# Optimization experiments

Hardware: AMD Instinct MI355X
Metric: run time of the kernel (lower is better)

The kernel has to match this reference:

```python
import jax, jax.numpy as jnp
import numpy as np


def _pairwise_dist(A, B):
    # Euclidean cdist via ||a||^2 + ||b||^2 - 2 a.b, avoiding a [B,N,M,D] intermediate.
    a2 = jnp.sum(A * A, axis=-1)  # [b, n]
    b2 = jnp.sum(B * B, axis=-1)  # [b, m]
    ab = jnp.einsum('bnd,bmd->bnm', A, B)  # [b, n, m]
    sq = a2[:, :, None] + b2[:, None, :] - 2.0 * ab
    return jnp.sqrt(jnp.maximum(sq, 0.0))


def setup_inputs() -> dict:
    key = jax.random.key(0)
    kA, kB = jax.random.split(key)
    A = jax.random.normal(kA, (4, 8192, 3), dtype=jnp.float32)
    B = jax.random.normal(kB, (4, 8192, 3), dtype=jnp.float32)
    return {"A": A, "B": B}


def reference(A, B):
    d = _pairwise_dist(A, B)              # [b, n, m]
    min_a2b = jnp.min(d, axis=2)          # [b, n]
    min_b2a = jnp.min(d, axis=1)          # [b, m]
    chamfer = jnp.mean(min_a2b, axis=1) + jnp.mean(min_b2a, axis=1)  # [b]
    return jnp.mean(chamfer) / 12.8
```

## Files before the change

### kernel.cpp

```cpp
#include <hip/hip_runtime.h>


typedef __bf16 bf16x8 __attribute__((ext_vector_type(8)));
typedef float f32x16 __attribute__((ext_vector_type(16)));
typedef unsigned short u16;

constexpr int NB = 4;
constexpr int NPTS = 8192;
constexpr int NROWS = 2 * NB * NPTS;
constexpr int FRAGS = 8;
constexpr int ROWS_PER_BLK = FRAGS * 32;
constexpr int ROWBLKS = NPTS / ROWS_PER_BLK;
constexpr int SSPLIT = 4;
constexpr int SPTS = NPTS / SSPLIT;
constexpr int TILES_PER_WAVE = SPTS / 32 / 4;
constexpr int DEPTH = 4;

constexpr size_t REST_OFF = 2u << 20;
constexpr size_t WSMIN_OFF = 4u << 20;

__device__ __forceinline__ float bsplit(float x, u16& hbits, float& hf) {
    unsigned u = __float_as_uint(x);
    unsigned r = (u + 0x7FFFu + ((u >> 16) & 1u)) & 0xFFFF0000u;
    hbits = (u16)(r >> 16);
    hf = __uint_as_float(r);
    return x - hf;
}

__global__ __launch_bounds__(256)
void chamfer_prep_kernel(const float* __restrict__ A, const float* __restrict__ B,
                         u16* __restrict__ streamT, u16* __restrict__ resT,
                         unsigned int* __restrict__ ws_min) {
    int idx = blockIdx.x * 256 + threadIdx.x;
    int pt = idx & (NPTS - 1);
    int batch = (idx >> 13) & (NB - 1);
    int set = idx >> 15;
    const float* src = (set ? B : A) + ((size_t)batch * NPTS + pt) * 3;
    float x = src[0], y = src[1], z = src[2];
    float s2 = fmaf(x, x, fmaf(y, y, z * z));
    float hf, h2;
    u16 s2h, s2l, s2ll, xh, xl, yh, yl, zh, zl, mxh, mxl, myh, myl, mzh, mzl;
    float r1 = bsplit(s2, s2h, hf);
    float r2 = bsplit(r1, s2l, h2);
    bsplit(r2, s2ll, h2);
    float t;
    t = bsplit(x, xh, hf);          bsplit(t, xl, h2);
    t = bsplit(y, yh, hf);          bsplit(t, yl, h2);
    t = bsplit(z, zh, hf);          bsplit(t, zl, h2);
    t = bsplit(-2.0f * x, mxh, hf); bsplit(t, mxl, h2);
    t = bsplit(-2.0f * y, myh, hf); bsplit(t, myl, h2);
    t = bsplit(-2.0f * z, mzh, hf); bsplit(t, mzl, h2);
    const unsigned ONE = 0x3F80u;
    #define PK(a, b) ((unsigned)(a) | ((unsigned)(b) << 16))
    uint4 rw0 = make_uint4(PK(s2h, s2l), PK(s2ll, ONE), PK(ONE, ONE), PK(mxh, myh));
    uint4 rw1 = make_uint4(PK(mzh, mxh), PK(myh, mzh), PK(mxl, myl), PK(mzl, 0));
    uint4 cw0 = make_uint4(PK(ONE, ONE), PK(ONE, s2h), PK(s2l, s2ll), PK(xh, yh));
    uint4 cw1 = make_uint4(PK(zh, xl), PK(yl, zl), PK(xh, yh), PK(zh, 0));
    #undef PK
    uint4* sp = (uint4*)(streamT + (size_t)idx * 16);
    uint4* rp = (uint4*)(resT + (size_t)idx * 16);
    sp[0] = rw0; sp[1] = rw1;
    rp[0] = cw0; rp[1] = cw1;
    ws_min[idx] = 0xFFFFFFFFu;
}

__device__ __forceinline__ float tree16acc(const f32x16& d, float acc) {
    float m0 = fminf(fminf(d[0],  d[1]),  d[2]);
    float m1 = fminf(fminf(d[3],  d[4]),  d[5]);
    float m2 = fminf(fminf(d[6],  d[7]),  d[8]);
    float m3 = fminf(fminf(d[9],  d[10]), d[11]);
    float m4 = fminf(fminf(d[12], d[13]), d[14]);
    float n0 = fminf(fminf(m0, m1), m2);
    float n1 = fminf(fminf(m3, m4), d[15]);
    return fminf(fminf(n0, n1), acc);
}

__global__ __launch_bounds__(256, 4)
void chamfer_minmfma_kernel(const u16* __restrict__ streamT,
                            const u16* __restrict__ resT,
                            unsigned int* __restrict__ ws_min) {
    int db     = blockIdx.x & 7;
    int rest   = blockIdx.x >> 3;
    int split  = rest & (SSPLIT - 1);
    int rowblk = rest >> 2;
    int batch  = db & (NB - 1);
    int dir    = db >> 2;

    int lane = threadIdx.x & 63;
    int wave = threadIdx.x >> 6;
    int l31 = lane & 31, lh = lane >> 5;

    const u16* rbase = resT + (((size_t)(dir * NB + batch) * NPTS) + rowblk * ROWS_PER_BLK) * 16;
    bf16x8 res0 = *(const bf16x8*)(rbase + (0 * 32 + l31) * 16 + lh * 8);
    bf16x8 res1 = *(const bf16x8*)(rbase + (1 * 32 + l31) * 16 + lh * 8);
    bf16x8 res2 = *(const bf16x8*)(rbase + (2 * 32 + l31) * 16 + lh * 8);
    bf16x8 res3 = *(const bf16x8*)(rbase + (3 * 32 + l31) * 16 + lh * 8);
    bf16x8 res4 = *(const bf16x8*)(rbase + (4 * 32 + l31) * 16 + lh * 8);
    bf16x8 res5 = *(const bf16x8*)(rbase + (5 * 32 + l31) * 16 + lh * 8);
    bf16x8 res6 = *(const bf16x8*)(rbase + (6 * 32 + l31) * 16 + lh * 8);
    bf16x8 res7 = *(const bf16x8*)(rbase + (7 * 32 + l31) * 16 + lh * 8);

    const uint4* wp = (const uint4*)streamT
                    + (size_t)((dir ^ 1) * NB + batch) * NPTS * 2
                    + (size_t)split * SPTS * 2
                    + (size_t)wave * TILES_PER_WAVE * 64
                    + (l31 * 2 + lh);

    f32x16 zf;
    #pragma unroll
    for (int j = 0; j < 16; ++j) zf[j] = 0.0f;
    float acc0 = 3.0e38f, acc1 = 3.0e38f, acc2 = 3.0e38f, acc3 = 3.0e38f;
    float acc4 = 3.0e38f, acc5 = 3.0e38f, acc6 = 3.0e38f, acc7 = 3.0e38f;

    uint4 pipe[DEPTH];
    #pragma unroll
    for (int i = 0; i < DEPTH; ++i) pipe[i] = wp[i * 64];

    for (int t = 0; t < TILES_PER_WAVE; t += DEPTH) {
        #pragma unroll
        for (int u = 0; u < DEPTH; ++u) {
            uint4 cur = pipe[u];
            pipe[u] = wp[(t + u + DEPTH) * 64];
            bf16x8 aop = __builtin_bit_cast(bf16x8, cur);
            f32x16 dA = __builtin_amdgcn_mfma_f32_32x32x16_bf16(aop, res0, zf, 0, 0, 0);
            f32x16 dB = __builtin_amdgcn_mfma_f32_32x32x16_bf16(aop, res1, zf, 0, 0, 0);
            acc0 = tree16acc(dA, acc0);
            dA = __builtin_amdgcn_mfma_f32_32x32x16_bf16(aop, res2, zf, 0, 0, 0);
            acc1 = tree16acc(dB, acc1);
            dB = __builtin_amdgcn_mfma_f32_32x32x16_bf16(aop, res3, zf, 0, 0, 0);
            acc2 = tree16acc(dA, acc2);
            dA = __builtin_amdgcn_mfma_f32_32x32x16_bf16(aop, res4, zf, 0, 0, 0);
            acc3 = tree16acc(dB, acc3);
            dB = __builtin_amdgcn_mfma_f32_32x32x16_bf16(aop, res5, zf, 0, 0, 0);
            acc4 = tree16acc(dA, acc4);
            dA = __builtin_amdgcn_mfma_f32_32x32x16_bf16(aop, res6, zf, 0, 0, 0);
            acc5 = tree16acc(dB, acc5);
            dB = __builtin_amdgcn_mfma_f32_32x32x16_bf16(aop, res7, zf, 0, 0, 0);
            acc6 = tree16acc(dA, acc6);
            acc7 = tree16acc(dB, acc7);
        }
    }

    unsigned int* wout = ws_min + (size_t)(dir * NB + batch) * NPTS + rowblk * ROWS_PER_BLK;
    float accs[FRAGS] = {acc0, acc1, acc2, acc3, acc4, acc5, acc6, acc7};
    #pragma unroll
    for (int f = 0; f < FRAGS; ++f) {
        float v = fminf(accs[f], __shfl_xor(accs[f], 32, 64));
        v = fmaxf(v, 0.0f);
        if (lh == 0) atomicMin(&wout[f * 32 + l31], __float_as_uint(v));
    }
}

__global__ __launch_bounds__(256)
void chamfer_reduce_kernel(const unsigned int* __restrict__ ws_min,
                           float* __restrict__ out) {
    constexpr float SCALE = 1.0f / (NB * NPTS * 12.8f);
    int idx = (blockIdx.x * 256 + threadIdx.x) * 4;
    uint4 v = *(const uint4*)(ws_min + idx);
    float s = sqrtf(__uint_as_float(v.x)) + sqrtf(__uint_as_float(v.y))
            + sqrtf(__uint_as_float(v.z)) + sqrtf(__uint_as_float(v.w));
    #pragma unroll
    for (int off = 32; off >= 1; off >>= 1) s += __shfl_down(s, off, 64);
    __shared__ float redl[4];
    if ((threadIdx.x & 63) == 0) redl[threadIdx.x >> 6] = s;
    __syncthreads();
    if (threadIdx.x == 0)
        atomicAdd(out, (redl[0] + redl[1] + redl[2] + redl[3]) * SCALE);
}

extern "C" void kernel_launch(void* const* d_in, const int* in_sizes, int n_in,
                              void* d_out, int out_size, void* d_ws, size_t ws_size,
                              hipStream_t stream) {
    const float* A = (const float*)d_in[0];
    const float* B = (const float*)d_in[1];
    float* out = (float*)d_out;
    u16* streamT = (u16*)d_ws;
    u16* resT = (u16*)((char*)d_ws + REST_OFF);
    unsigned int* wsm = (unsigned int*)((char*)d_ws + WSMIN_OFF);

    hipMemsetAsync(d_out, 0, sizeof(float), stream);
    chamfer_prep_kernel<<<NROWS / 256, 256, 0, stream>>>(A, B, streamT, resT, wsm);
    chamfer_minmfma_kernel<<<2 * NB * ROWBLKS * SSPLIT, 256, 0, stream>>>(streamT, resT, wsm);
    chamfer_reduce_kernel<<<NROWS / 4 / 256, 256, 0, stream>>>(wsm, out);
}
```

Measured before the change: 33.73 us.

## Fuse min-reduction and final sum into MFMA kernel, drop split and memset

```diff
diff --git a/kernel.cpp b/kernel.cpp
--- a/kernel.cpp
+++ b/kernel.cpp
@@ -8,16 +8,14 @@
 constexpr int NB = 4;
 constexpr int NPTS = 8192;
 constexpr int NROWS = 2 * NB * NPTS;
-constexpr int FRAGS = 8;
+constexpr int FRAGS = 4;
 constexpr int ROWS_PER_BLK = FRAGS * 32;
 constexpr int ROWBLKS = NPTS / ROWS_PER_BLK;
-constexpr int SSPLIT = 4;
-constexpr int SPTS = NPTS / SSPLIT;
-constexpr int TILES_PER_WAVE = SPTS / 32 / 4;
+constexpr int TILES = NPTS / 32;
+constexpr int TILES_PER_WAVE = TILES / 4;
 constexpr int DEPTH = 4;
 
 constexpr size_t REST_OFF = 2u << 20;
-constexpr size_t WSMIN_OFF = 4u << 20;
 
 __device__ __forceinline__ float bsplit(float x, u16& hbits, float& hf) {
     unsigned u = __float_as_uint(x);
@@ -30,8 +28,9 @@
 __global__ __launch_bounds__(256)
 void chamfer_prep_kernel(const float* __restrict__ A, const float* __restrict__ B,
                          u16* __restrict__ streamT, u16* __restrict__ resT,
-                         unsigned int* __restrict__ ws_min) {
+                         float* __restrict__ out) {
     int idx = blockIdx.x * 256 + threadIdx.x;
+    if (idx == 0) out[0] = 0.0f;
     int pt = idx & (NPTS - 1);
     int batch = (idx >> 13) & (NB - 1);
     int set = idx >> 15;
@@ -61,7 +60,6 @@
     uint4* rp = (uint4*)(resT + (size_t)idx * 16);
     sp[0] = rw0; sp[1] = rw1;
     rp[0] = cw0; rp[1] = cw1;
-    ws_min[idx] = 0xFFFFFFFFu;
 }
 
 __device__ __forceinline__ float tree16acc(const f32x16& d, float acc) {
@@ -78,11 +76,10 @@
 __global__ __launch_bounds__(256, 4)
 void chamfer_minmfma_kernel(const u16* __restrict__ streamT,
                             const u16* __restrict__ resT,
-                            unsigned int* __restrict__ ws_min) {
+                            float* __restrict__ out) {
+    constexpr float SCALE = 1.0f / (NB * NPTS * 12.8f);
     int db     = blockIdx.x & 7;
-    int rest   = blockIdx.x >> 3;
-    int split  = rest & (SSPLIT - 1);
-    int rowblk = rest >> 2;
+    int rowblk = blockIdx.x >> 3;
     int batch  = db & (NB - 1);
     int dir    = db >> 2;
 
@@ -95,14 +92,9 @@
     bf16x8 res1 = *(const bf16x8*)(rbase + (1 * 32 + l31) * 16 + lh * 8);
     bf16x8 res2 = *(const bf16x8*)(rbase + (2 * 32 + l31) * 16 + lh * 8);
     bf16x8 res3 = *(const bf16x8*)(rbase + (3 * 32 + l31) * 16 + lh * 8);
-    bf16x8 res4 = *(const bf16x8*)(rbase + (4 * 32 + l31) * 16 + lh * 8);
-    bf16x8 res5 = *(const bf16x8*)(rbase + (5 * 32 + l31) * 16 + lh * 8);
-    bf16x8 res6 = *(const bf16x8*)(rbase + (6 * 32 + l31) * 16 + lh * 8);
-    bf16x8 res7 = *(const bf16x8*)(rbase + (7 * 32 + l31) * 16 + lh * 8);
 
     const uint4* wp = (const uint4*)streamT
                     + (size_t)((dir ^ 1) * NB + batch) * NPTS * 2
-                    + (size_t)split * SPTS * 2
                     + (size_t)wave * TILES_PER_WAVE * 64
                     + (l31 * 2 + lh);
 
@@ -110,7 +102,6 @@
     #pragma unroll
     for (int j = 0; j < 16; ++j) zf[j] = 0.0f;
     float acc0 = 3.0e38f, acc1 = 3.0e38f, acc2 = 3.0e38f, acc3 = 3.0e38f;
-    float acc4 = 3.0e38f, acc5 = 3.0e38f, acc6 = 3.0e38f, acc7 = 3.0e38f;
 
     uint4 pipe[DEPTH];
     #pragma unroll
@@ -129,43 +120,34 @@
             acc1 = tree16acc(dB, acc1);
             dB = __builtin_amdgcn_mfma_f32_32x32x16_bf16(aop, res3, zf, 0, 0, 0);
             acc2 = tree16acc(dA, acc2);
-            dA = __builtin_amdgcn_mfma_f32_32x32x16_bf16(aop, res4, zf, 0, 0, 0);
             acc3 = tree16acc(dB, acc3);
-            dB = __builtin_amdgcn_mfma_f32_32x32x16_bf16(aop, res5, zf, 0, 0, 0);
-            acc4 = tree16acc(dA, acc4);
-            dA = __builtin_amdgcn_mfma_f32_32x32x16_bf16(aop, res6, zf, 0, 0, 0);
-            acc5 = tree16acc(dB, acc5);
-            dB = __builtin_amdgcn_mfma_f32_32x32x16_bf16(aop, res7, zf, 0, 0, 0);
-            acc6 = tree16acc(dA, acc6);
-            acc7 = tree16acc(dB, acc7);
         }
     }
 
-    unsigned int* wout = ws_min + (size_t)(dir * NB + batch) * NPTS + rowblk * ROWS_PER_BLK;
-    float accs[FRAGS] = {acc0, acc1, acc2, acc3, acc4, acc5, acc6, acc7};
+    float accs[FRAGS] = {acc0, acc1, acc2, acc3};
     #pragma unroll
-    for (int f = 0; f < FRAGS; ++f) {
-        float v = fminf(accs[f], __shfl_xor(accs[f], 32, 64));
-        v = fmaxf(v, 0.0f);
-        if (lh == 0) atomicMin(&wout[f * 32 + l31], __float_as_uint(v));
+    for (int f = 0; f < FRAGS; ++f)
+        accs[f] = fminf(accs[f], __shfl_xor(accs[f], 32, 64));
+
+    __shared__ float part[4][ROWS_PER_BLK];
+    __shared__ float red[2];
+    if (lh == 0) {
+        #pragma unroll
+        for (int f = 0; f < FRAGS; ++f) part[wave][f * 32 + l31] = accs[f];
     }
-}
-
-__global__ __launch_bounds__(256)
-void chamfer_reduce_kernel(const unsigned int* __restrict__ ws_min,
-                           float* __restrict__ out) {
-    constexpr float SCALE = 1.0f / (NB * NPTS * 12.8f);
-    int idx = (blockIdx.x * 256 + threadIdx.x) * 4;
-    uint4 v = *(const uint4*)(ws_min + idx);
-    float s = sqrtf(__uint_as_float(v.x)) + sqrtf(__uint_as_float(v.y))
-            + sqrtf(__uint_as_float(v.z)) + sqrtf(__uint_as_float(v.w));
-    #pragma unroll
-    for (int off = 32; off >= 1; off >>= 1) s += __shfl_down(s, off, 64);
-    __shared__ float redl[4];
-    if ((threadIdx.x & 63) == 0) redl[threadIdx.x >> 6] = s;
     __syncthreads();
-    if (threadIdx.x == 0)
-        atomicAdd(out, (redl[0] + redl[1] + redl[2] + redl[3]) * SCALE);
+    int tid = threadIdx.x;
+    if (tid < ROWS_PER_BLK) {
+        float m = fminf(fminf(part[0][tid], part[1][tid]),
+                        fminf(part[2][tid], part[3][tid]));
+        float s = sqrtf(fmaxf(m, 0.0f));
+        #pragma unroll
+        for (int off = 32; off >= 1; off >>= 1)
+            s += __shfl_down(s, off, 64);
+        if ((tid & 63) == 0) red[tid >> 6] = s;
+    }
+    __syncthreads();
+    if (tid == 0) atomicAdd(out, (red[0] + red[1]) * SCALE);
 }
 
 extern "C" void kernel_launch(void* const* d_in, const int* in_sizes, int n_in,
@@ -176,10 +158,7 @@
     float* out = (float*)d_out;
     u16* streamT = (u16*)d_ws;
     u16* resT = (u16*)((char*)d_ws + REST_OFF);
-    unsigned int* wsm = (unsigned int*)((char*)d_ws + WSMIN_OFF);
 
-    hipMemsetAsync(d_out, 0, sizeof(float), stream);
-    chamfer_prep_kernel<<<NROWS / 256, 256, 0, stream>>>(A, B, streamT, resT, wsm);
-    chamfer_minmfma_kernel<<<2 * NB * ROWBLKS * SSPLIT, 256, 0, stream>>>(streamT, resT, wsm);
-    chamfer_reduce_kernel<<<NROWS / 4 / 256, 256, 0, stream>>>(wsm, out);
+    chamfer_prep_kernel<<<NROWS / 256, 256, 0, stream>>>(A, B, streamT, resT, out);
+    chamfer_minmfma_kernel<<<2 * NB * ROWBLKS, 256, 0, stream>>>(streamT, resT, out);
 }
```

Measured after the change: 50.74 us. 1.5x slower.
